# Optimization experiments

Hardware: AMD Instinct MI355X
Metric: run time of the kernel (lower is better)

## Reference

```python
import jax, jax.numpy as jnp
import numpy as np

B, S, D, H = 4, 2048, 2048, 16
HD = D // H  # 128


def _rope(t, cos, sin):
    # t: [B, S, H, HD]; cos/sin: [S, HD//2]
    tr = t.reshape(t.shape[:-1] + (HD // 2, 2))
    t1, t2 = tr[..., 0], tr[..., 1]
    c = cos[None, :, None, :]
    s = sin[None, :, None, :]
    o1 = t1 * c - t2 * s
    o2 = t1 * s + t2 * c
    return jnp.stack([o1, o2], axis=-1).reshape(t.shape)


def setup_inputs() -> dict:
    key = jax.random.key(0)
    ks = jax.random.split(key, 9)
    init_std = HD ** -0.5
    pos = jnp.arange(S, dtype=jnp.float32)[:, None]
    inv = 1.0 / (10000.0 ** (jnp.arange(0, HD, 2, dtype=jnp.float32) / HD))
    ang = pos * inv[None, :]
    return {
        "x": jax.random.normal(ks[0], (B, S, D), jnp.float32),
        "query": jax.random.normal(ks[1], (B, S, D), jnp.float32),
        "value": jax.random.normal(ks[2], (B, S, D), jnp.float32),
        "freqs_cos": jnp.cos(ang),
        "freqs_sin": jnp.sin(ang),
        "key_w": jax.random.normal(ks[3], (D, D), jnp.float32) * init_std,
        "key_b": jnp.zeros((D,), jnp.float32),
        "proj_w": jax.random.normal(ks[4], (D, D), jnp.float32) * init_std,
        "proj_b": jnp.zeros((D,), jnp.float32),
    }


def reference(x, query, value, freqs_cos, freqs_sin, key_w, key_b, proj_w, proj_b):
    # key projection applied to x; query/value arrive pre-projected
    k = (jnp.einsum("bsd,ed->bse", x, key_w) + key_b).reshape(B, S, H, HD)
    q = query.reshape(B, S, H, HD)
    v = value.reshape(B, S, H, HD)
    q = _rope(q, freqs_cos, freqs_sin)
    k = _rope(k, freqs_cos, freqs_sin)
    scale = 1.0 / np.sqrt(HD)
    scores = jnp.einsum("bqhd,bkhd->bhqk", q, k) * scale  # [B,H,S,S]
    causal = jnp.tril(jnp.ones((S, S), bool))
    scores = jnp.where(causal[None, None], scores, jnp.finfo(scores.dtype).min)
    probs = jax.nn.softmax(scores, axis=-1)
    out = jnp.einsum("bhqk,bkhd->bqhd", probs, v).reshape(B, S, D)
    return jnp.einsum("bsd,ed->bse", out, proj_w) + proj_b
```

## Files before the change

kernel.cpp:

```cpp
#include <hip/hip_runtime.h>
#include <hip/hip_bf16.h>
#include <stdint.h>

#define BB 4
#define SS 2048
#define DD 2048
#define HH 16
#define HD 128
#define MTOT (BB*SS)

typedef __attribute__((ext_vector_type(8))) short short8;
typedef __attribute__((ext_vector_type(4))) float f32x4;

__device__ __forceinline__ unsigned short f2bf(float f) {
    union { float f; unsigned int u; } v; v.f = f;
    unsigned int u = v.u;
    return (unsigned short)((u + 0x7FFFu + ((u >> 16) & 1u)) >> 16);
}
__device__ __forceinline__ unsigned short f2bf_ru(float f) {
    union { float f; unsigned int u; } v; v.f = f;
    return (unsigned short)((v.u + 0x8000u) >> 16);
}

__global__ __launch_bounds__(256) void convert_kernel(
    const float* __restrict__ src, unsigned short* __restrict__ dst, int n4) {
    int i = blockIdx.x * 256 + threadIdx.x;
    if (i >= n4) return;
    float4 v = ((const float4*)src)[i];
    unsigned int lo = (unsigned int)f2bf(v.x) | ((unsigned int)f2bf(v.y) << 16);
    unsigned int hi = (unsigned int)f2bf(v.z) | ((unsigned int)f2bf(v.w) << 16);
    ((uint2*)dst)[i] = make_uint2(lo, hi);
}

__global__ __launch_bounds__(256) void rope_q_kernel(
    const float* __restrict__ q, const float* __restrict__ fc,
    const float* __restrict__ fs, unsigned short* __restrict__ dst) {
    int idx = blockIdx.x * 256 + threadIdx.x;
    int row   = idx >> 10;
    int s     = row & (SS - 1);
    int p     = idx & 63;
    float2 t = ((const float2*)q)[idx];
    float c = fc[s*64 + p], sn = fs[s*64 + p];
    float o1 = t.x*c - t.y*sn;
    float o2 = t.x*sn + t.y*c;
    ((unsigned int*)dst)[idx] = (unsigned int)f2bf(o1) | ((unsigned int)f2bf(o2) << 16);
}

__global__ __launch_bounds__(256) void transpose_v_kernel(
    const float* __restrict__ v, unsigned short* __restrict__ vt) {
    __shared__ unsigned short tile[64][72];
    int bh = blockIdx.z;
    int s0 = blockIdx.x * 64, d0 = blockIdx.y * 64;
    int t = threadIdx.x;
    #pragma unroll
    for (int it = 0; it < 4; ++it) {
        int i  = it*16 + (t >> 4);
        int j4 = t & 15;
        float4 f = *(const float4*)(v +
            (((size_t)((bh >> 4)*SS + s0 + i)*HH + (bh & 15))*HD + d0 + j4*4));
        unsigned int lo = (unsigned int)f2bf(f.x) | ((unsigned int)f2bf(f.y) << 16);
        unsigned int hi = (unsigned int)f2bf(f.z) | ((unsigned int)f2bf(f.w) << 16);
        *(uint2*)&tile[i][j4*4] = make_uint2(lo, hi);
    }
    __syncthreads();
    unsigned int* vt32 = (unsigned int*)vt;
    #pragma unroll
    for (int it = 0; it < 8; ++it) {
        int task = it*256 + t;
        int tt = task & 31;
        int d  = task >> 5;
        int slo = ((tt & 1) << 5) + (tt >> 1);
        unsigned int lo = tile[slo][d], hi = tile[slo + 16][d];
        vt32[((size_t)bh*HD + d0 + d)*(SS/2) + (s0 >> 1) + tt] = lo | (hi << 16);
    }
}

template<int MODE>
__global__ __launch_bounds__(256, 2) void gemm_kernel(
    const unsigned short* __restrict__ A, const unsigned short* __restrict__ W,
    const float* __restrict__ bias, const float* __restrict__ fc,
    const float* __restrict__ fs, void* __restrict__ out)
{
    __shared__ unsigned short As[128*32];
    __shared__ unsigned short Bs[128*32];
    const int K = DD;
    int L   = blockIdx.y * 16 + blockIdx.x;
    int swz = (L & 7) * 128 + (L >> 3);
    int m0 = (swz >> 4) * 128, n0 = (swz & 15) * 128;
    int t = threadIdx.x, lane = t & 63, w = t >> 6;
    int wm = w >> 1, wn = w & 1;
    int l15 = lane & 15, quad = lane >> 4;

    f32x4 acc[4][4] = {};

    for (int k0 = 0; k0 < K; k0 += 32) {
        __syncthreads();
        #pragma unroll
        for (int i = 0; i < 2; ++i) {
            int ci  = i*256 + t;
            int row = ci >> 2;
            int ce  = (ci & 3) * 8;
            const unsigned short* ga = A + (size_t)(m0 + row) * K + k0 + ce;
            const unsigned short* gb = W + (size_t)(n0 + row) * K + k0 + ce;
            unsigned short* la = As + (size_t)(i*256 + w*64) * 8;
            unsigned short* lb = Bs + (size_t)(i*256 + w*64) * 8;
            __builtin_amdgcn_global_load_lds(
                (__attribute__((address_space(1))) void*)(uintptr_t)ga,
                (__attribute__((address_space(3))) void*)la, 16, 0, 0);
            __builtin_amdgcn_global_load_lds(
                (__attribute__((address_space(1))) void*)(uintptr_t)gb,
                (__attribute__((address_space(3))) void*)lb, 16, 0, 0);
        }
        __syncthreads();

        short8 af[4], bw[4];
        #pragma unroll
        for (int i = 0; i < 4; ++i) {
            af[i] = *(const short8*)(As + (size_t)(wm*64 + i*16 + l15)*32 + quad*8);
            bw[i] = *(const short8*)(Bs + (size_t)(wn*64 + i*16 + l15)*32 + quad*8);
        }
        #pragma unroll
        for (int i = 0; i < 4; ++i)
            #pragma unroll
            for (int j = 0; j < 4; ++j)
                acc[i][j] = __builtin_amdgcn_mfma_f32_16x16x32_bf16(
                    af[i], bw[j], acc[i][j], 0, 0, 0);
    }

    #pragma unroll
    for (int i = 0; i < 4; ++i) {
        #pragma unroll
        for (int j = 0; j < 4; ++j) {
            int col = n0 + wn*64 + j*16 + l15;
            float bv = bias[col];
            #pragma unroll
            for (int r = 0; r < 4; ++r) {
                int row = m0 + wm*64 + i*16 + quad*4 + r;
                float v = acc[i][j][r] + bv;
                if (MODE == 0) {
                    int s = row & (SS - 1);
                    int p = (col & 127) >> 1;
                    float other = __shfl_xor(v, 1);
                    float c = fc[s*64 + p], sn = fs[s*64 + p];
                    float res = (col & 1) ? (other*sn + v*c) : (v*c - other*sn);
                    ((unsigned short*)out)[(size_t)row*DD + col] = f2bf(res);
                } else {
                    ((float*)out)[(size_t)row*DD + col] = v;
                }
            }
        }
    }
}

__global__ __launch_bounds__(512, 4) void attn_kernel(
    const unsigned short* __restrict__ Q, const unsigned short* __restrict__ Kr,
    const unsigned short* __restrict__ Vt, unsigned short* __restrict__ O)
{
    constexpr int PSTR = 72;
    __shared__ unsigned short Ks[2*64*128];
    __shared__ unsigned short VTs[2*128*64];
    __shared__ unsigned short Ps[128*PSTR];

    int L   = blockIdx.y * 8 + blockIdx.x;
    int swz = (L & 7) * 64 + (L >> 3);
    int bh   = swz >> 3;
    int pair = swz & 7;

    int b = bh >> 4, h = bh & 15;
    size_t base  = (size_t)b*SS*DD + (size_t)h*HD;
    size_t vbase = (size_t)bh*HD*SS;

    int t = threadIdx.x, lane = t & 63, w = t >> 6;
    int l15 = lane & 15, quad = lane >> 4;
    int l7 = l15 & 7;

    const float scl2 = 0.08838834764831845f * 1.44269504088896f;

    auto stage = [&](int jt, int buf) {
        int j0s = jt * 64;
        #pragma unroll
        for (int i = 0; i < 2; ++i) {
            int ci  = i*512 + t;
            int row = ci >> 4;
            int cc  = ci & 15;
            int gch = cc ^ (row & 7);
            const unsigned short* ga = Kr + base + (size_t)(j0s + row)*DD + gch*8;
            unsigned short* la = Ks + buf*(64*128) + (size_t)(i*512 + w*64)*8;
            __builtin_amdgcn_global_load_lds(
                (__attribute__((address_space(1))) void*)(uintptr_t)ga,
                (__attribute__((address_space(3))) void*)la, 16, 0, 0);
        }
        #pragma unroll
        for (int i = 0; i < 2; ++i) {
            int ci  = i*512 + t;
            int d   = ci >> 3;
            int cc  = ci & 7;
            int gch = cc ^ (d & 7);
            const unsigned short* ga = Vt + vbase + (size_t)d*SS + j0s + gch*8;
            unsigned short* la = VTs + buf*(128*64) + (size_t)(i*512 + w*64)*8;
            __builtin_amdgcn_global_load_lds(
                (__attribute__((address_space(1))) void*)(uintptr_t)ga,
                (__attribute__((address_space(3))) void*)la, 16, 0, 0);
        }
    };

    for (int ph = 0; ph < 2; ++ph) {
        int qt = ph ? (15 - pair) : pair;
        int q0 = qt * 128;
        int rw = q0 + w*16;

        short8 aq[4];
        #pragma unroll
        for (int kk = 0; kk < 4; ++kk)
            aq[kk] = *(const short8*)(Q + base +
                (size_t)(rw + l15)*DD + kk*32 + quad*8);

        float m_i[4], l_i[4];
        #pragma unroll
        for (int r = 0; r < 4; ++r) { m_i[r] = -1e30f; l_i[r] = 0.f; }
        f32x4 o_acc[8] = {};

        __syncthreads();
        stage(0, 0);
        int jmax = 2*qt + 1;

        for (int jt = 0; jt <= jmax; ++jt) {
            int pb = jt & 1;
            int j0 = jt * 64;
            const unsigned short* Kb = Ks  + pb*(64*128);
            const unsigned short* Vb = VTs + pb*(128*64);

            __syncthreads();
            if (jt < jmax) stage(jt + 1, pb ^ 1);

            if (j0 > rw + 15) continue;

            f32x4 sacc[4];
            #pragma unroll
            for (int c = 0; c < 4; ++c) {
                sacc[c] = (f32x4){0.f, 0.f, 0.f, 0.f};
                #pragma unroll
                for (int kk = 0; kk < 4; ++kk) {
                    short8 bk = *(const short8*)(Kb +
                        (size_t)(c*16 + l15)*128 + ((kk*4 + quad) ^ l7)*8);
                    sacc[c] = __builtin_amdgcn_mfma_f32_16x16x32_bf16(aq[kk], bk, sacc[c], 0,0,0);
                }
            }

            bool diag = (j0 + 63 > rw);
            float pp[4][4], mt4[4];
            #pragma unroll
            for (int r = 0; r < 4; ++r) mt4[r] = -1e30f;
            #pragma unroll
            for (int c = 0; c < 4; ++c)
                #pragma unroll
                for (int r = 0; r < 4; ++r) {
                    float v = sacc[c][r] * scl2;
                    if (diag) {
                        int cg = j0 + c*16 + l15;
                        int rg = rw + quad*4 + r;
                        if (cg > rg) v = -1e30f;
                    }
                    pp[c][r] = v;
                    mt4[r] = fmaxf(mt4[r], v);
                }

            bool grow = false;
            #pragma unroll
            for (int r = 0; r < 4; ++r) {
                float m = mt4[r];
                m = fmaxf(m, __shfl_xor(m, 1));
                m = fmaxf(m, __shfl_xor(m, 2));
                m = fmaxf(m, __shfl_xor(m, 4));
                m = fmaxf(m, __shfl_xor(m, 8));
                mt4[r] = m;
                grow = grow || (m > m_i[r] + 8.0f);
            }
            if (__any(grow)) {
                #pragma unroll
                for (int r = 0; r < 4; ++r) {
                    float mn = fmaxf(m_i[r], mt4[r]);
                    float a  = exp2f(m_i[r] - mn);
                    m_i[r] = mn;
                    l_i[r] *= a;
                    mt4[r] = a;
                }
                #pragma unroll
                for (int f = 0; f < 8; ++f)
                    #pragma unroll
                    for (int r = 0; r < 4; ++r)
                        o_acc[f][r] *= mt4[r];
            }

            float rs[4];
            #pragma unroll
            for (int r = 0; r < 4; ++r) {
                float e0 = exp2f(pp[0][r] - m_i[r]);
                float e1 = exp2f(pp[1][r] - m_i[r]);
                float e2 = exp2f(pp[2][r] - m_i[r]);
                float e3 = exp2f(pp[3][r] - m_i[r]);
                rs[r] = (e0 + e1) + (e2 + e3);
                unsigned int lo = (unsigned int)f2bf_ru(e0) | ((unsigned int)f2bf_ru(e1) << 16);
                unsigned int hi = (unsigned int)f2bf_ru(e2) | ((unsigned int)f2bf_ru(e3) << 16);
                *(uint2*)&Ps[(size_t)(w*16 + quad*4 + r)*PSTR + l15*4] = make_uint2(lo, hi);
            }
            #pragma unroll
            for (int r = 0; r < 4; ++r) {
                float s = rs[r];
                s += __shfl_xor(s, 1);
                s += __shfl_xor(s, 2);
                s += __shfl_xor(s, 4);
                s += __shfl_xor(s, 8);
                l_i[r] += s;
            }

            #pragma unroll
            for (int kk2 = 0; kk2 < 2; ++kk2) {
                short8 ap = *(const short8*)(Ps + (size_t)(w*16 + l15)*PSTR + kk2*32 + quad*8);
                #pragma unroll
                for (int f = 0; f < 8; ++f) {
                    short8 bv = *(const short8*)(Vb +
                        (size_t)(f*16 + l15)*64 + ((kk2*4 + quad) ^ l7)*8);
                    o_acc[f] = __builtin_amdgcn_mfma_f32_16x16x32_bf16(ap, bv, o_acc[f], 0,0,0);
                }
            }
        }

        #pragma unroll
        for (int f = 0; f < 8; ++f) {
            #pragma unroll
            for (int r = 0; r < 4; ++r) {
                int srow = rw + quad*4 + r;
                int d = f*16 + l15;
                O[base + (size_t)srow*DD + d] = f2bf(o_acc[f][r] / l_i[r]);
            }
        }
    }
}

extern "C" void kernel_launch(void* const* d_in, const int* in_sizes, int n_in,
                              void* d_out, int out_size, void* d_ws, size_t ws_size,
                              hipStream_t stream) {
    const float* x      = (const float*)d_in[0];
    const float* query  = (const float*)d_in[1];
    const float* value  = (const float*)d_in[2];
    const float* fc     = (const float*)d_in[3];
    const float* fs     = (const float*)d_in[4];
    const float* key_w  = (const float*)d_in[5];
    const float* key_b  = (const float*)d_in[6];
    const float* proj_w = (const float*)d_in[7];
    const float* proj_b = (const float*)d_in[8];

    const int ND  = BB*SS*DD;
    const int NW  = DD*DD;
    unsigned short* xb  = (unsigned short*)d_ws;
    unsigned short* kwb = xb  + ND;
    unsigned short* pwb = kwb + NW;
    unsigned short* qr  = pwb + NW;
    unsigned short* vt  = qr  + ND;
    unsigned short* kr  = vt  + ND;
    unsigned short* ao  = xb;

    convert_kernel<<<ND/4/256, 256, 0, stream>>>(x, xb, ND/4);
    convert_kernel<<<NW/4/256, 256, 0, stream>>>(key_w, kwb, NW/4);
    convert_kernel<<<NW/4/256, 256, 0, stream>>>(proj_w, pwb, NW/4);
    rope_q_kernel<<<ND/2/256, 256, 0, stream>>>(query, fc, fs, qr);
    transpose_v_kernel<<<dim3(SS/64, HD/64, BB*HH), 256, 0, stream>>>(value, vt);

    dim3 gg(DD/128, MTOT/128);
    gemm_kernel<0><<<gg, 256, 0, stream>>>(xb, kwb, key_b, fc, fs, (void*)kr);
    attn_kernel<<<dim3(8, BB*HH), 512, 0, stream>>>(qr, kr, vt, ao);
    gemm_kernel<1><<<gg, 256, 0, stream>>>(ao, pwb, proj_b, nullptr, nullptr, d_out);
}
```

Before: 592.0 us.

## Single-buffer V with late wait, fold softmax scale into Q rope, defer row-sum reduction

V is now single-buffered and loaded at the start of each KV tile, with a partial vmcnt wait and barrier placed just before the PV MFMAs. This lets the V load overlap the QK and softmax work and frees LDS, which may allow higher occupancy. The softmax scale is folded into the Q rope kernel so the per-score multiply disappears. The row-sum shuffle reduction is moved out of the loop to a single reduction at the end, and the final division becomes a reciprocal multiply. Risks are the hand-written vmcnt counting, the extra barrier per iteration, and a small precision change from scaling Q before the bf16 rounding.

```diff
diff --git a/kernel.cpp b/kernel.cpp
--- a/kernel.cpp
+++ b/kernel.cpp
@@ -35,14 +35,15 @@
 __global__ __launch_bounds__(256) void rope_q_kernel(
     const float* __restrict__ q, const float* __restrict__ fc,
     const float* __restrict__ fs, unsigned short* __restrict__ dst) {
+    const float scl2 = 0.08838834764831845f * 1.44269504088896f;
     int idx = blockIdx.x * 256 + threadIdx.x;
     int row   = idx >> 10;
     int s     = row & (SS - 1);
     int p     = idx & 63;
     float2 t = ((const float2*)q)[idx];
     float c = fc[s*64 + p], sn = fs[s*64 + p];
-    float o1 = t.x*c - t.y*sn;
-    float o2 = t.x*sn + t.y*c;
+    float o1 = (t.x*c - t.y*sn) * scl2;
+    float o2 = (t.x*sn + t.y*c) * scl2;
     ((unsigned int*)dst)[idx] = (unsigned int)f2bf(o1) | ((unsigned int)f2bf(o2) << 16);
 }
 
@@ -158,7 +159,7 @@
 {
     constexpr int PSTR = 72;
     __shared__ unsigned short Ks[2*64*128];
-    __shared__ unsigned short VTs[2*128*64];
+    __shared__ unsigned short VTs[128*64];
     __shared__ unsigned short Ps[128*PSTR];
 
     int L   = blockIdx.y * 8 + blockIdx.x;
@@ -174,9 +175,7 @@
     int l15 = lane & 15, quad = lane >> 4;
     int l7 = l15 & 7;
 
-    const float scl2 = 0.08838834764831845f * 1.44269504088896f;
-
-    auto stage = [&](int jt, int buf) {
+    auto stageK = [&](int jt, int buf) {
         int j0s = jt * 64;
         #pragma unroll
         for (int i = 0; i < 2; ++i) {
@@ -190,6 +189,9 @@
                 (__attribute__((address_space(1))) void*)(uintptr_t)ga,
                 (__attribute__((address_space(3))) void*)la, 16, 0, 0);
         }
+    };
+    auto stageV = [&](int jt) {
+        int j0s = jt * 64;
         #pragma unroll
         for (int i = 0; i < 2; ++i) {
             int ci  = i*512 + t;
@@ -197,7 +199,7 @@
             int cc  = ci & 7;
             int gch = cc ^ (d & 7);
             const unsigned short* ga = Vt + vbase + (size_t)d*SS + j0s + gch*8;
-            unsigned short* la = VTs + buf*(128*64) + (size_t)(i*512 + w*64)*8;
+            unsigned short* la = VTs + (size_t)(i*512 + w*64)*8;
             __builtin_amdgcn_global_load_lds(
                 (__attribute__((address_space(1))) void*)(uintptr_t)ga,
                 (__attribute__((address_space(3))) void*)la, 16, 0, 0);
@@ -215,124 +217,130 @@
             aq[kk] = *(const short8*)(Q + base +
                 (size_t)(rw + l15)*DD + kk*32 + quad*8);
 
-        float m_i[4], l_i[4];
-        #pragma unroll
-        for (int r = 0; r < 4; ++r) { m_i[r] = -1e30f; l_i[r] = 0.f; }
+        float m_i[4], l_lane[4];
+        #pragma unroll
+        for (int r = 0; r < 4; ++r) { m_i[r] = -1e30f; l_lane[r] = 0.f; }
         f32x4 o_acc[8] = {};
 
         __syncthreads();
-        stage(0, 0);
+        stageK(0, 0);
         int jmax = 2*qt + 1;
 
         for (int jt = 0; jt <= jmax; ++jt) {
             int pb = jt & 1;
             int j0 = jt * 64;
-            const unsigned short* Kb = Ks  + pb*(64*128);
-            const unsigned short* Vb = VTs + pb*(128*64);
+            const unsigned short* Kb = Ks + pb*(64*128);
 
             __syncthreads();
-            if (jt < jmax) stage(jt + 1, pb ^ 1);
-
-            if (j0 > rw + 15) continue;
-
-            f32x4 sacc[4];
+            stageV(jt);
+            __builtin_amdgcn_sched_barrier(0);
+            if (jt < jmax) stageK(jt + 1, pb ^ 1);
+
+            bool active = (j0 <= rw + 15);
+            if (active) {
+                f32x4 sacc[4];
+                #pragma unroll
+                for (int c = 0; c < 4; ++c) {
+                    sacc[c] = (f32x4){0.f, 0.f, 0.f, 0.f};
+                    #pragma unroll
+                    for (int kk = 0; kk < 4; ++kk) {
+                        short8 bk = *(const short8*)(Kb +
+                            (size_t)(c*16 + l15)*128 + ((kk*4 + quad) ^ l7)*8);
+                        sacc[c] = __builtin_amdgcn_mfma_f32_16x16x32_bf16(aq[kk], bk, sacc[c], 0,0,0);
+                    }
+                }
+
+                bool diag = (j0 + 63 > rw);
+                float pp[4][4], mt4[4];
+                #pragma unroll
+                for (int c = 0; c < 4; ++c)
+                    #pragma unroll
+                    for (int r = 0; r < 4; ++r) {
+                        float v = sacc[c][r];
+                        if (diag) {
+                            int cg = j0 + c*16 + l15;
+                            int rg = rw + quad*4 + r;
+                            if (cg > rg) v = -1e30f;
+                        }
+                        pp[c][r] = v;
+                    }
+                #pragma unroll
+                for (int r = 0; r < 4; ++r)
+                    mt4[r] = fmaxf(fmaxf(pp[0][r], pp[1][r]), fmaxf(pp[2][r], pp[3][r]));
+
+                bool grow = false;
+                #pragma unroll
+                for (int r = 0; r < 4; ++r) {
+                    float m = mt4[r];
+                    m = fmaxf(m, __shfl_xor(m, 1));
+                    m = fmaxf(m, __shfl_xor(m, 2));
+                    m = fmaxf(m, __shfl_xor(m, 4));
+                    m = fmaxf(m, __shfl_xor(m, 8));
+                    mt4[r] = m;
+                    grow = grow || (m > m_i[r] + 8.0f);
+                }
+                if (__any(grow)) {
+                    #pragma unroll
+                    for (int r = 0; r < 4; ++r) {
+                        float mn = fmaxf(m_i[r], mt4[r]);
+                        float a  = exp2f(m_i[r] - mn);
+                        m_i[r] = mn;
+                        l_lane[r] *= a;
+                        mt4[r] = a;
+                    }
+                    #pragma unroll
+                    for (int f = 0; f < 8; ++f)
+                        #pragma unroll
+                        for (int r = 0; r < 4; ++r)
+                            o_acc[f][r] *= mt4[r];
+                }
+
+                #pragma unroll
+                for (int r = 0; r < 4; ++r) {
+                    float e0 = exp2f(pp[0][r] - m_i[r]);
+                    float e1 = exp2f(pp[1][r] - m_i[r]);
+                    float e2 = exp2f(pp[2][r] - m_i[r]);
+                    float e3 = exp2f(pp[3][r] - m_i[r]);
+                    l_lane[r] += (e0 + e1) + (e2 + e3);
+                    unsigned int lo = (unsigned int)f2bf_ru(e0) | ((unsigned int)f2bf_ru(e1) << 16);
+                    unsigned int hi = (unsigned int)f2bf_ru(e2) | ((unsigned int)f2bf_ru(e3) << 16);
+                    *(uint2*)&Ps[(size_t)(w*16 + quad*4 + r)*PSTR + l15*4] = make_uint2(lo, hi);
+                }
+            }
+
+            __builtin_amdgcn_sched_barrier(0);
+            if (jt < jmax) { asm volatile("s_waitcnt vmcnt(2)" ::: "memory"); }
+            else           { asm volatile("s_waitcnt vmcnt(0)" ::: "memory"); }
+            __builtin_amdgcn_s_barrier();
+            __builtin_amdgcn_sched_barrier(0);
+
+            if (active) {
+                #pragma unroll
+                for (int kk2 = 0; kk2 < 2; ++kk2) {
+                    short8 ap = *(const short8*)(Ps + (size_t)(w*16 + l15)*PSTR + kk2*32 + quad*8);
+                    #pragma unroll
+                    for (int f = 0; f < 8; ++f) {
+                        short8 bv = *(const short8*)(VTs +
+                            (size_t)(f*16 + l15)*64 + ((kk2*4 + quad) ^ l7)*8);
+                        o_acc[f] = __builtin_amdgcn_mfma_f32_16x16x32_bf16(ap, bv, o_acc[f], 0,0,0);
+                    }
+                }
+            }
+        }
+
+        #pragma unroll
+        for (int r = 0; r < 4; ++r) {
+            float s = l_lane[r];
+            s += __shfl_xor(s, 1);
+            s += __shfl_xor(s, 2);
+            s += __shfl_xor(s, 4);
+            s += __shfl_xor(s, 8);
+            float inv = 1.0f / s;
+            int srow = rw + quad*4 + r;
             #pragma unroll
-            for (int c = 0; c < 4; ++c) {
-                sacc[c] = (f32x4){0.f, 0.f, 0.f, 0.f};
-                #pragma unroll
-                for (int kk = 0; kk < 4; ++kk) {
-                    short8 bk = *(const short8*)(Kb +
-                        (size_t)(c*16 + l15)*128 + ((kk*4 + quad) ^ l7)*8);
-                    sacc[c] = __builtin_amdgcn_mfma_f32_16x16x32_bf16(aq[kk], bk, sacc[c], 0,0,0);
-                }
-            }
-
-            bool diag = (j0 + 63 > rw);
-            float pp[4][4], mt4[4];
-            #pragma unroll
-            for (int r = 0; r < 4; ++r) mt4[r] = -1e30f;
-            #pragma unroll
-            for (int c = 0; c < 4; ++c)
-                #pragma unroll
-                for (int r = 0; r < 4; ++r) {
-                    float v = sacc[c][r] * scl2;
-                    if (diag) {
-                        int cg = j0 + c*16 + l15;
-                        int rg = rw + quad*4 + r;
-                        if (cg > rg) v = -1e30f;
-                    }
-                    pp[c][r] = v;
-                    mt4[r] = fmaxf(mt4[r], v);
-                }
-
-            bool grow = false;
-            #pragma unroll
-            for (int r = 0; r < 4; ++r) {
-                float m = mt4[r];
-                m = fmaxf(m, __shfl_xor(m, 1));
-                m = fmaxf(m, __shfl_xor(m, 2));
-                m = fmaxf(m, __shfl_xor(m, 4));
-                m = fmaxf(m, __shfl_xor(m, 8));
-                mt4[r] = m;
-                grow = grow || (m > m_i[r] + 8.0f);
-            }
-            if (__any(grow)) {
-                #pragma unroll
-                for (int r = 0; r < 4; ++r) {
-                    float mn = fmaxf(m_i[r], mt4[r]);
-                    float a  = exp2f(m_i[r] - mn);
-                    m_i[r] = mn;
-                    l_i[r] *= a;
-                    mt4[r] = a;
-                }
-                #pragma unroll
-                for (int f = 0; f < 8; ++f)
-                    #pragma unroll
-                    for (int r = 0; r < 4; ++r)
-                        o_acc[f][r] *= mt4[r];
-            }
-
-            float rs[4];
-            #pragma unroll
-            for (int r = 0; r < 4; ++r) {
-                float e0 = exp2f(pp[0][r] - m_i[r]);
-                float e1 = exp2f(pp[1][r] - m_i[r]);
-                float e2 = exp2f(pp[2][r] - m_i[r]);
-                float e3 = exp2f(pp[3][r] - m_i[r]);
-                rs[r] = (e0 + e1) + (e2 + e3);
-                unsigned int lo = (unsigned int)f2bf_ru(e0) | ((unsigned int)f2bf_ru(e1) << 16);
-                unsigned int hi = (unsigned int)f2bf_ru(e2) | ((unsigned int)f2bf_ru(e3) << 16);
-                *(uint2*)&Ps[(size_t)(w*16 + quad*4 + r)*PSTR + l15*4] = make_uint2(lo, hi);
-            }
-            #pragma unroll
-            for (int r = 0; r < 4; ++r) {
-                float s = rs[r];
-                s += __shfl_xor(s, 1);
-                s += __shfl_xor(s, 2);
-                s += __shfl_xor(s, 4);
-                s += __shfl_xor(s, 8);
-                l_i[r] += s;
-            }
-
-            #pragma unroll
-            for (int kk2 = 0; kk2 < 2; ++kk2) {
-                short8 ap = *(const short8*)(Ps + (size_t)(w*16 + l15)*PSTR + kk2*32 + quad*8);
-                #pragma unroll
-                for (int f = 0; f < 8; ++f) {
-                    short8 bv = *(const short8*)(Vb +
-                        (size_t)(f*16 + l15)*64 + ((kk2*4 + quad) ^ l7)*8);
-                    o_acc[f] = __builtin_amdgcn_mfma_f32_16x16x32_bf16(ap, bv, o_acc[f], 0,0,0);
-                }
-            }
-        }
-
-        #pragma unroll
-        for (int f = 0; f < 8; ++f) {
-            #pragma unroll
-            for (int r = 0; r < 4; ++r) {
-                int srow = rw + quad*4 + r;
+            for (int f = 0; f < 8; ++f) {
                 int d = f*16 + l15;
-                O[base + (size_t)srow*DD + d] = f2bf(o_acc[f][r] / l_i[r]);
+                O[base + (size_t)srow*DD + d] = f2bf(o_acc[f][r] * inv);
             }
         }
     }
```

Result: faster. 565.0 us (-4.6%).
